# Kernel tuning notes

Measured on AMD Instinct MI355X. Metric: run time of the kernel, lower is better.

## Reference

```python
import jax, jax.numpy as jnp
import numpy as np

B, S, D, H, HD, F = 8, 1024, 512, 8, 64, 2048
EPS = 1e-6

def rmsnorm(x, w):
    var = jnp.mean(x * x, axis=-1, keepdims=True)
    return w * (x * jax.lax.rsqrt(var + EPS))

def setup_inputs() -> dict:
    key = jax.random.key(0)
    ks = jax.random.split(key, 10)
    sd = 512 ** -0.5
    return {
        "primals_1": jax.random.normal(ks[0], (D, D), jnp.float32) * sd,
        "primals_2": jax.random.normal(ks[1], (D, D), jnp.float32) * sd,
        "primals_3": jax.random.normal(ks[2], (D, D), jnp.float32) * sd,
        "primals_4": jax.random.normal(ks[3], (D, D), jnp.float32) * sd,
        "primals_5": jax.random.uniform(ks[4], (D,), jnp.float32, 0.5, 1.5),
        "primals_6": jax.random.normal(ks[5], (F, D), jnp.float32) * sd,
        "primals_7": jax.random.normal(ks[6], (D, F), jnp.float32) * (F ** -0.5),
        "primals_8": jax.random.uniform(ks[7], (D,), jnp.float32, 0.5, 1.5),
        "primals_9": jax.random.normal(ks[8], (B, S, D), jnp.float32),
        "primals_10": jax.random.normal(ks[9], (B, H, S, S), jnp.float32) * 0.1,
    }

def reference(primals_1, primals_2, primals_3, primals_4, primals_5,
              primals_6, primals_7, primals_8, primals_9, primals_10):
    x = primals_9
    # --- self-attention sublayer ---
    h = rmsnorm(x, primals_5)                      # [B,S,D]
    # T5: no 1/sqrt(head_dim) scaling
    q = (h @ primals_3.T).reshape(B, S, H, HD).transpose(0, 2, 1, 3)  # [B,H,S,HD]
    k = (h @ primals_1.T).reshape(B, S, H, HD).transpose(0, 2, 1, 3)
    v = (h @ primals_4.T).reshape(B, S, H, HD).transpose(0, 2, 1, 3)
    scores = jnp.einsum('bhqd,bhkd->bhqk', q, k) + primals_10        # [B,H,S,S]
    attn = jax.nn.softmax(scores, axis=-1)
    ctx = jnp.einsum('bhqk,bhkd->bhqd', attn, v)                     # [B,H,S,HD]
    ctx = ctx.transpose(0, 2, 1, 3).reshape(B, S, D)
    x = x + ctx @ primals_2.T                       # residual add_1
    # --- FFN sublayer ---
    h2 = rmsnorm(x, primals_8)
    ff = jax.nn.relu(h2 @ primals_6.T)              # [B,S,F]
    out = x + ff @ primals_7.T                      # add_3
    return out
```

## Files before the change

### kernel.cpp

```cpp
#include <hip/hip_runtime.h>

#define B_ 8
#define S_ 1024
#define D_ 512
#define H_ 8
#define HD_ 64
#define F_ 2048

typedef unsigned short u16;
typedef unsigned int u32;
typedef __attribute__((ext_vector_type(8))) short bf16x8;
typedef __attribute__((ext_vector_type(4))) float f32x4;

__device__ __forceinline__ float bf2f(u16 u) {
  union { unsigned int i; float f; } v; v.i = ((unsigned int)u) << 16; return v.f;
}
__device__ __forceinline__ u16 f2bf(float f) {
  union { float f; unsigned int i; } v; v.f = f;
  unsigned int r = v.i + 0x7fffu + ((v.i >> 16) & 1u);
  return (u16)(r >> 16);
}

__device__ __forceinline__ void gl2lds16(const u16* g, u16* lds) {
  __builtin_amdgcn_global_load_lds(
      (const __attribute__((address_space(1))) unsigned int*)g,
      (__attribute__((address_space(3))) unsigned int*)lds, 16, 0, 0);
}

__global__ __launch_bounds__(256) void cvt_w_k(const float* __restrict__ wq, const float* __restrict__ wk,
                                               const float* __restrict__ wv, const float* __restrict__ wo,
                                               const float* __restrict__ wf1, const float* __restrict__ wf2,
                                               u16* __restrict__ dst) {
  size_t gid = (size_t)blockIdx.x * 256 + threadIdx.x;
  size_t e0 = gid * 4;
  const float* src; size_t loc;
  if      (e0 <  262144) { src = wq;  loc = e0; }
  else if (e0 <  524288) { src = wk;  loc = e0 -  262144; }
  else if (e0 <  786432) { src = wv;  loc = e0 -  524288; }
  else if (e0 < 1048576) { src = wo;  loc = e0 -  786432; }
  else if (e0 < 2097152) { src = wf1; loc = e0 - 1048576; }
  else                   { src = wf2; loc = e0 - 2097152; }
  float4 v = *(const float4*)(src + loc);
  ushort4 o; o.x = f2bf(v.x); o.y = f2bf(v.y); o.z = f2bf(v.z); o.w = f2bf(v.w);
  *(ushort4*)(dst + e0) = o;
}

template <int IN_BF16>
__global__ __launch_bounds__(256) void rmsnorm_k(const void* __restrict__ xv,
                                                 const float* __restrict__ w,
                                                 u16* __restrict__ out) {
  int row = blockIdx.x;
  int tid = threadIdx.x;
  float x0, x1;
  if (IN_BF16) {
    u32 v = ((const u32*)((const u16*)xv + (size_t)row * D_))[tid];
    x0 = bf2f((u16)(v & 0xffffu)); x1 = bf2f((u16)(v >> 16));
  } else {
    float2 v = ((const float2*)((const float*)xv + (size_t)row * D_))[tid];
    x0 = v.x; x1 = v.y;
  }
  float s = x0 * x0 + x1 * x1;
#pragma unroll
  for (int off = 32; off >= 1; off >>= 1) s += __shfl_xor(s, off, 64);
  __shared__ float red[4];
  int lane = tid & 63, wid = tid >> 6;
  if (lane == 0) red[wid] = s;
  __syncthreads();
  float tot = red[0] + red[1] + red[2] + red[3];
  float inv = rsqrtf(tot * (1.0f / D_) + 1e-6f);
  float2 wv = ((const float2*)w)[tid];
  u32 o = (u32)f2bf(x0 * inv * wv.x) | ((u32)f2bf(x1 * inv * wv.y) << 16);
  ((u32*)(out + (size_t)row * D_))[tid] = o;
}

template <int RELU, int RMODE, int OF32, int BM>
__global__ __launch_bounds__(256) void gemm_mfma_k(const u16* __restrict__ A,
                                                   const u16* __restrict__ W,
                                                   const void* __restrict__ Rv,
                                                   void* __restrict__ Cv,
                                                   int M, int N, int K) {
  constexpr int MI  = BM / 32;
  constexpr int ACH = BM / 16;
  __shared__ __align__(16) u16 As[BM * 32];
  __shared__ __align__(16) u16 Bs[128 * 32];
  int tid = threadIdx.x;
  int w = tid >> 6, l = tid & 63;
  int quad = l >> 4, l16 = l & 15;
  int m0 = blockIdx.y * BM, n0 = blockIdx.x * 128;
  int wr = (w >> 1) * (BM / 2), wc = (w & 1) * 64;

  int c_sw = (l & 3) ^ ((l >> 2) & 3);
  int r_in = l >> 2;
  int swz = quad ^ (l16 & 3);

  f32x4 acc[MI][4];
#pragma unroll
  for (int i = 0; i < MI; i++)
#pragma unroll
    for (int j = 0; j < 4; j++) acc[i][j] = (f32x4)(0.0f);

  for (int k0 = 0; k0 < K; k0 += 32) {
    __syncthreads();
#pragma unroll
    for (int t = 0; t < (ACH + 8) / 4; t++) {
      int ch = w * ((ACH + 8) / 4) + t;
      const u16* src; u16* dst;
      if (ch < ACH) { src = A + (size_t)(m0 + ch * 16 + r_in) * K;         dst = As + ch * 512; }
      else          { src = W + (size_t)(n0 + (ch - ACH) * 16 + r_in) * K; dst = Bs + (ch - ACH) * 512; }
      gl2lds16(src + k0 + c_sw * 8, dst);
    }
    __syncthreads();
    bf16x8 af[MI], bf[4];
#pragma unroll
    for (int i = 0; i < MI; i++)
      af[i] = *(const bf16x8*)(As + (wr + i * 16 + l16) * 32 + swz * 8);
#pragma unroll
    for (int j = 0; j < 4; j++)
      bf[j] = *(const bf16x8*)(Bs + (wc + j * 16 + l16) * 32 + swz * 8);
#pragma unroll
    for (int i = 0; i < MI; i++)
#pragma unroll
      for (int j = 0; j < 4; j++)
        acc[i][j] = __builtin_amdgcn_mfma_f32_16x16x32_bf16(af[i], bf[j], acc[i][j], 0, 0, 0);
  }

#pragma unroll
  for (int i = 0; i < MI; i++)
#pragma unroll
    for (int r = 0; r < 4; r++) {
      int mrow = m0 + wr + i * 16 + quad * 4 + r;
      size_t base = (size_t)mrow * N + n0 + wc + l16;
#pragma unroll
      for (int j = 0; j < 4; j++) {
        float v = acc[i][j][r];
        if (RELU) v = fmaxf(v, 0.0f);
        if (RMODE == 1) v += ((const float*)Rv)[base + j * 16];
        if (RMODE == 2) v += bf2f(((const u16*)Rv)[base + j * 16]);
        if (OF32) ((float*)Cv)[base + j * 16] = v;
        else      ((u16*)Cv)[base + j * 16]   = f2bf(v);
      }
    }
}

__global__ __launch_bounds__(256) void transpose_v_k(const u16* __restrict__ qkv,
                                                     u16* __restrict__ vt) {
  __shared__ u16 T[64][72];
  int t = threadIdx.x;
  int s0 = blockIdx.x * 64, h = blockIdx.y, b = blockIdx.z;
  int skey = t >> 3, dch = (t & 7) * 8;
  int rot = dch >> 3;
#pragma unroll
  for (int rnd = 0; rnd < 2; rnd++) {
    int s = s0 + skey + rnd * 32;
    bf16x8 vv = *(const bf16x8*)(qkv + ((size_t)(b * S_) + s) * 1536 + 1024 + h * HD_ + dch);
#pragma unroll
    for (int i = 0; i < 8; i++) {
      int ii = (i + rot) & 7;
      T[dch + ii][skey + rnd * 32] = (u16)((short*)&vv)[ii];
    }
  }
  __syncthreads();
  int d = t >> 2, kc = (t & 3) * 16;
  bf16x8 a0 = *(const bf16x8*)(&T[d][kc]);
  bf16x8 a1 = *(const bf16x8*)(&T[d][kc + 8]);
  u16* dst = vt + ((size_t)(b * H_ + h) * HD_ + d) * S_ + s0 + kc;
  *(bf16x8*)dst       = a0;
  *(bf16x8*)(dst + 8) = a1;
}

#define FIXED_M 20.0f

__global__ __launch_bounds__(256, 2) void attn_v9_k(const u16* __restrict__ qkv,
                                                    const u16* __restrict__ vt,
                                                    const float* __restrict__ bias,
                                                    u16* __restrict__ ctx) {
  int tid = threadIdx.x;
  int w = tid >> 6, lane = tid & 63;
  int quad = lane >> 4, l16 = lane & 15;
  int h = blockIdx.y, b = blockIdx.z;
  int q0 = blockIdx.x * 64;

  __shared__ __align__(16) u16 KV[2][4 * 2048];
  __shared__ __align__(16) u16 BiasL[2][4][2048];
  __shared__ __align__(16) u16 Pl[4][16 * 72];

  const u16* qrow = qkv + ((size_t)(b * S_) + q0 + w * 16 + l16) * 1536 + h * HD_;
  bf16x8 qf0 = *(const bf16x8*)(qrow + quad * 8);
  bf16x8 qf1 = *(const bf16x8*)(qrow + 32 + quad * 8);

  float lr = 0.0f;
  f32x4 Oacc[4];
#pragma unroll
  for (int nt = 0; nt < 4; nt++) Oacc[nt] = (f32x4)(0.0f);

  const float* brow0 = bias + ((size_t)((b * H_ + h) * S_) + q0 + w * 16) * S_;

  int kv_srow_base = lane >> 2;
  int kv_sc = lane & 3;
  int b_rl_base = lane >> 4;
  int b_p = lane & 15;

  auto stage = [&](u16* kvbuf, u16* bbuf, int kt) {
#pragma unroll
    for (int i = 0; i < 4; i++) {
      int srow = i * 16 + kv_srow_base;
      int slc = kv_sc ^ (srow & 3);
      const u16* src;
      if (w == 0)      src = qkv + ((size_t)(b * S_) + kt + srow) * 1536 + 512 + h * HD_ + slc * 8;
      else if (w == 1) src = qkv + ((size_t)(b * S_) + kt + srow) * 1536 + 544 + h * HD_ + slc * 8;
      else if (w == 2) src = vt + ((size_t)((b * H_ + h) * HD_) + srow) * S_ + kt + slc * 8;
      else             src = vt + ((size_t)((b * H_ + h) * HD_) + srow) * S_ + kt + 32 + slc * 8;
      gl2lds16(src, kvbuf + w * 2048 + i * 512);
    }
#pragma unroll
    for (int i = 0; i < 4; i++) {
      int rl = i * 4 + b_rl_base;
      int c = b_p ^ (rl & 7);
      const float* fsrc = brow0 + (size_t)rl * S_ + kt + c * 4;
      gl2lds16((const u16*)fsrc, bbuf + i * 512);
    }
  };

  stage(&KV[0][0], &BiasL[0][w][0], 0);
  __syncthreads();

  int cur = 0;
#pragma unroll 1
  for (int t = 0; t < 16; t++) {
    int kt = t * 64;
    if (t < 15) stage(&KV[cur ^ 1][0], &BiasL[cur ^ 1][w][0], kt + 64);
    const u16* kvb = &KV[cur][0];
    const u16* bb = &BiasL[cur][w][0];

    f32x4 sg[4];
    __builtin_amdgcn_s_setprio(1);
#pragma unroll
    for (int g = 0; g < 4; g++) {
      int row = g * 16 + l16;
      int sw = quad ^ (row & 3);
      bf16x8 kf0 = *(const bf16x8*)(kvb + row * 32 + sw * 8);
      bf16x8 kf1 = *(const bf16x8*)(kvb + 2048 + row * 32 + sw * 8);
      f32x4 a = (f32x4)(0.0f);
      a = __builtin_amdgcn_mfma_f32_16x16x32_bf16(kf0, qf0, a, 0, 0, 0);
      a = __builtin_amdgcn_mfma_f32_16x16x32_bf16(kf1, qf1, a, 0, 0, 0);
      sg[g] = a;
    }
    __builtin_amdgcn_s_setprio(0);

#pragma unroll
    for (int g = 0; g < 4; g++) {
      f32x4 bf4 = *(const f32x4*)(bb + (size_t)l16 * 128 + ((u32)((g * 4 + quad) ^ (l16 & 7))) * 8);
      float p0 = __expf(sg[g][0] + bf4[0] - FIXED_M);
      float p1 = __expf(sg[g][1] + bf4[1] - FIXED_M);
      float p2 = __expf(sg[g][2] + bf4[2] - FIXED_M);
      float p3 = __expf(sg[g][3] + bf4[3] - FIXED_M);
      lr += (p0 + p1) + (p2 + p3);
      ushort4 pw;
      pw.x = f2bf(p0); pw.y = f2bf(p1); pw.z = f2bf(p2); pw.w = f2bf(p3);
      *(ushort4*)(&Pl[w][l16 * 72 + g * 16 + quad * 4]) = pw;
    }

    bf16x8 pf0 = *(const bf16x8*)(&Pl[w][l16 * 72 + quad * 8]);
    bf16x8 pf1 = *(const bf16x8*)(&Pl[w][l16 * 72 + 32 + quad * 8]);

    __builtin_amdgcn_s_setprio(1);
#pragma unroll
    for (int nt = 0; nt < 4; nt++) {
      int row = nt * 16 + l16;
      int sw = quad ^ (row & 3);
      bf16x8 vf0 = *(const bf16x8*)(kvb + 4096 + row * 32 + sw * 8);
      bf16x8 vf1 = *(const bf16x8*)(kvb + 6144 + row * 32 + sw * 8);
      Oacc[nt] = __builtin_amdgcn_mfma_f32_16x16x32_bf16(pf0, vf0, Oacc[nt], 0, 0, 0);
      Oacc[nt] = __builtin_amdgcn_mfma_f32_16x16x32_bf16(pf1, vf1, Oacc[nt], 0, 0, 0);
    }
    __builtin_amdgcn_s_setprio(0);

    if (t < 15) {
      asm volatile("s_waitcnt vmcnt(0)" ::: "memory");
      __builtin_amdgcn_sched_barrier(0);
      __builtin_amdgcn_s_barrier();
    }
    cur ^= 1;
  }

  float s = lr;
  s += __shfl_xor(s, 16, 64);
  s += __shfl_xor(s, 32, 64);
  size_t obase = ((size_t)(b * S_) + q0 + w * 16) * D_ + h * HD_;
#pragma unroll
  for (int r = 0; r < 4; r++) {
    float inv = 1.0f / __shfl(s, quad * 4 + r, 64);
    int qr = quad * 4 + r;
#pragma unroll
    for (int nt = 0; nt < 4; nt++) {
      ctx[obase + (size_t)qr * D_ + nt * 16 + l16] = f2bf(Oacc[nt][r] * inv);
    }
  }
}

extern "C" void kernel_launch(void* const* d_in, const int* in_sizes, int n_in,
                              void* d_out, int out_size, void* d_ws, size_t ws_size,
                              hipStream_t stream) {
  const float* Wk   = (const float*)d_in[0];
  const float* Wo   = (const float*)d_in[1];
  const float* Wq   = (const float*)d_in[2];
  const float* Wv   = (const float*)d_in[3];
  const float* g1   = (const float*)d_in[4];
  const float* Wf1  = (const float*)d_in[5];
  const float* Wf2  = (const float*)d_in[6];
  const float* g2   = (const float*)d_in[7];
  const float* X    = (const float*)d_in[8];
  const float* bias = (const float*)d_in[9];
  float* out = (float*)d_out;

  const size_t MD = (size_t)B_ * S_ * D_;
  u16* wbf   = (u16*)d_ws;
  u16* Wqkvb = wbf;
  u16* Wob   = wbf +  786432;
  u16* Wf1b  = wbf + 1048576;
  u16* Wf2b  = wbf + 2097152;
  u16* h     = wbf + 3145728;
  u16* qkv   = h + MD;
  u16* vtb   = qkv + 3 * MD;
  u16* ctx   = vtb + MD;
  u16* ff    = ctx + MD;
  u16* x1    = qkv;
  u16* h2    = h;

  dim3 blk(256);
  const int M = B_ * S_;

  cvt_w_k<<<3072, blk, 0, stream>>>(Wq, Wk, Wv, Wo, Wf1, Wf2, wbf);

  rmsnorm_k<0><<<M, blk, 0, stream>>>(X, g1, h);

  dim3 gqkv(1536 / 128, M / 128);
  gemm_mfma_k<0, 0, 0, 128><<<gqkv, blk, 0, stream>>>(h, Wqkvb, nullptr, qkv, M, 1536, D_);

  dim3 gt(S_ / 64, H_, B_);
  transpose_v_k<<<gt, blk, 0, stream>>>(qkv, vtb);

  dim3 ga(S_ / 64, H_, B_);
  attn_v9_k<<<ga, blk, 0, stream>>>(qkv, vtb, bias, ctx);

  dim3 g512(D_ / 128, M / 128);
  gemm_mfma_k<0, 1, 0, 128><<<g512, blk, 0, stream>>>(ctx, Wob, X, x1, M, D_, D_);

  rmsnorm_k<1><<<M, blk, 0, stream>>>(x1, g2, h2);

  dim3 gff1(F_ / 128, M / 128);
  gemm_mfma_k<1, 0, 0, 128><<<gff1, blk, 0, stream>>>(h2, Wf1b, nullptr, ff, M, F_, D_);

  gemm_mfma_k<0, 2, 1, 128><<<g512, blk, 0, stream>>>(ff, Wf2b, x1, out, M, D_, F_);
}
```

Before: 567.9 us.

## Use 128-key attention tiles with shared K/V/bias staging and smaller GEMM M-tiles

The attention kernel now stages 128 keys per iteration instead of 64, so the loop runs 8 times with half as many barriers. All four waves cooperatively load K, V^T and the bias tiles into new XOR-swizzled LDS layouts, and each wave runs two 64-key sub-steps per tile. LDS use rises to about 115 KB per block, so launch bounds drop to one block per CU. The output-projection and FFN2 GEMMs switch to 64-row M tiles, doubling their grid to raise occupancy on the 512-wide outputs.

```diff
diff --git a/kernel.cpp b/kernel.cpp
--- a/kernel.cpp
+++ b/kernel.cpp
@@ -170,18 +170,19 @@
 
 #define FIXED_M 20.0f
 
-__global__ __launch_bounds__(256, 2) void attn_v9_k(const u16* __restrict__ qkv,
-                                                    const u16* __restrict__ vt,
-                                                    const float* __restrict__ bias,
-                                                    u16* __restrict__ ctx) {
+__global__ __launch_bounds__(256, 1) void attn_v10_k(const u16* __restrict__ qkv,
+                                                     const u16* __restrict__ vt,
+                                                     const float* __restrict__ bias,
+                                                     u16* __restrict__ ctx) {
   int tid = threadIdx.x;
   int w = tid >> 6, lane = tid & 63;
   int quad = lane >> 4, l16 = lane & 15;
   int h = blockIdx.y, b = blockIdx.z;
   int q0 = blockIdx.x * 64;
 
-  __shared__ __align__(16) u16 KV[2][4 * 2048];
-  __shared__ __align__(16) u16 BiasL[2][4][2048];
+  __shared__ __align__(16) u16 Ks[2][128 * 64];
+  __shared__ __align__(16) u16 Vs[2][64 * 128];
+  __shared__ __align__(16) u16 Bs[2][64 * 256];
   __shared__ __align__(16) u16 Pl[4][16 * 72];
 
   const u16* qrow = qkv + ((size_t)(b * S_) + q0 + w * 16 + l16) * 1536 + h * HD_;
@@ -193,93 +194,90 @@
 #pragma unroll
   for (int nt = 0; nt < 4; nt++) Oacc[nt] = (f32x4)(0.0f);
 
-  const float* brow0 = bias + ((size_t)((b * H_ + h) * S_) + q0 + w * 16) * S_;
-
-  int kv_srow_base = lane >> 2;
-  int kv_sc = lane & 3;
-  int b_rl_base = lane >> 4;
-  int b_p = lane & 15;
-
-  auto stage = [&](u16* kvbuf, u16* bbuf, int kt) {
+  auto stage = [&](int buf, int kt) {
 #pragma unroll
     for (int i = 0; i < 4; i++) {
-      int srow = i * 16 + kv_srow_base;
-      int slc = kv_sc ^ (srow & 3);
-      const u16* src;
-      if (w == 0)      src = qkv + ((size_t)(b * S_) + kt + srow) * 1536 + 512 + h * HD_ + slc * 8;
-      else if (w == 1) src = qkv + ((size_t)(b * S_) + kt + srow) * 1536 + 544 + h * HD_ + slc * 8;
-      else if (w == 2) src = vt + ((size_t)((b * H_ + h) * HD_) + srow) * S_ + kt + slc * 8;
-      else             src = vt + ((size_t)((b * H_ + h) * HD_) + srow) * S_ + kt + 32 + slc * 8;
-      gl2lds16(src, kvbuf + w * 2048 + i * 512);
+      int j = w * 4 + i;
+      int kr = j * 8 + (lane >> 3);
+      int cs = (lane & 7) ^ (lane >> 3);
+      const u16* src = qkv + ((size_t)(b * S_) + kt + kr) * 1536 + 512 + h * HD_ + cs * 8;
+      gl2lds16(src, &Ks[buf][j * 512]);
     }
 #pragma unroll
     for (int i = 0; i < 4; i++) {
-      int rl = i * 4 + b_rl_base;
-      int c = b_p ^ (rl & 7);
-      const float* fsrc = brow0 + (size_t)rl * S_ + kt + c * 4;
-      gl2lds16((const u16*)fsrc, bbuf + i * 512);
+      int j = w * 4 + i;
+      int vr = j * 4 + (lane >> 4);
+      int cs = (lane & 15) ^ (vr & 7);
+      const u16* src = vt + ((size_t)((b * H_ + h) * HD_) + vr) * S_ + kt + cs * 8;
+      gl2lds16(src, &Vs[buf][j * 512]);
+    }
+#pragma unroll
+    for (int i = 0; i < 8; i++) {
+      int rq = i * 2 + (lane >> 5);
+      int cs = (lane & 31) ^ (rq & 7);
+      const float* fsrc = bias + ((size_t)((b * H_ + h) * S_) + q0 + w * 16 + rq) * S_ + kt + cs * 4;
+      gl2lds16((const u16*)fsrc, &Bs[buf][(w * 16 + i * 2) * 256]);
     }
   };
 
-  stage(&KV[0][0], &BiasL[0][w][0], 0);
+  stage(0, 0);
   __syncthreads();
 
   int cur = 0;
 #pragma unroll 1
-  for (int t = 0; t < 16; t++) {
-    int kt = t * 64;
-    if (t < 15) stage(&KV[cur ^ 1][0], &BiasL[cur ^ 1][w][0], kt + 64);
-    const u16* kvb = &KV[cur][0];
-    const u16* bb = &BiasL[cur][w][0];
-
-    f32x4 sg[4];
-    __builtin_amdgcn_s_setprio(1);
-#pragma unroll
-    for (int g = 0; g < 4; g++) {
-      int row = g * 16 + l16;
-      int sw = quad ^ (row & 3);
-      bf16x8 kf0 = *(const bf16x8*)(kvb + row * 32 + sw * 8);
-      bf16x8 kf1 = *(const bf16x8*)(kvb + 2048 + row * 32 + sw * 8);
-      f32x4 a = (f32x4)(0.0f);
-      a = __builtin_amdgcn_mfma_f32_16x16x32_bf16(kf0, qf0, a, 0, 0, 0);
-      a = __builtin_amdgcn_mfma_f32_16x16x32_bf16(kf1, qf1, a, 0, 0, 0);
-      sg[g] = a;
-    }
-    __builtin_amdgcn_s_setprio(0);
-
-#pragma unroll
-    for (int g = 0; g < 4; g++) {
-      f32x4 bf4 = *(const f32x4*)(bb + (size_t)l16 * 128 + ((u32)((g * 4 + quad) ^ (l16 & 7))) * 8);
-      float p0 = __expf(sg[g][0] + bf4[0] - FIXED_M);
-      float p1 = __expf(sg[g][1] + bf4[1] - FIXED_M);
-      float p2 = __expf(sg[g][2] + bf4[2] - FIXED_M);
-      float p3 = __expf(sg[g][3] + bf4[3] - FIXED_M);
-      lr += (p0 + p1) + (p2 + p3);
-      ushort4 pw;
-      pw.x = f2bf(p0); pw.y = f2bf(p1); pw.z = f2bf(p2); pw.w = f2bf(p3);
-      *(ushort4*)(&Pl[w][l16 * 72 + g * 16 + quad * 4]) = pw;
-    }
-
-    bf16x8 pf0 = *(const bf16x8*)(&Pl[w][l16 * 72 + quad * 8]);
-    bf16x8 pf1 = *(const bf16x8*)(&Pl[w][l16 * 72 + 32 + quad * 8]);
-
-    __builtin_amdgcn_s_setprio(1);
-#pragma unroll
-    for (int nt = 0; nt < 4; nt++) {
-      int row = nt * 16 + l16;
-      int sw = quad ^ (row & 3);
-      bf16x8 vf0 = *(const bf16x8*)(kvb + 4096 + row * 32 + sw * 8);
-      bf16x8 vf1 = *(const bf16x8*)(kvb + 6144 + row * 32 + sw * 8);
-      Oacc[nt] = __builtin_amdgcn_mfma_f32_16x16x32_bf16(pf0, vf0, Oacc[nt], 0, 0, 0);
-      Oacc[nt] = __builtin_amdgcn_mfma_f32_16x16x32_bf16(pf1, vf1, Oacc[nt], 0, 0, 0);
-    }
-    __builtin_amdgcn_s_setprio(0);
-
-    if (t < 15) {
-      asm volatile("s_waitcnt vmcnt(0)" ::: "memory");
-      __builtin_amdgcn_sched_barrier(0);
-      __builtin_amdgcn_s_barrier();
-    }
+  for (int t = 0; t < 8; t++) {
+    int kt = t * 128;
+    if (t < 7) stage(cur ^ 1, kt + 128);
+    const u16* Ksb = &Ks[cur][0];
+    const u16* Vsb = &Vs[cur][0];
+    const float* Bsb = (const float*)&Bs[cur][0];
+
+#pragma unroll
+    for (int s = 0; s < 2; s++) {
+      f32x4 sg[4];
+      __builtin_amdgcn_s_setprio(1);
+#pragma unroll
+      for (int g = 0; g < 4; g++) {
+        int r = s * 64 + g * 16 + l16;
+        bf16x8 kf0 = *(const bf16x8*)(Ksb + r * 64 + ((quad ^ (l16 & 7)) * 8));
+        bf16x8 kf1 = *(const bf16x8*)(Ksb + r * 64 + (((4 + quad) ^ (l16 & 7)) * 8));
+        f32x4 a = (f32x4)(0.0f);
+        a = __builtin_amdgcn_mfma_f32_16x16x32_bf16(kf0, qf0, a, 0, 0, 0);
+        a = __builtin_amdgcn_mfma_f32_16x16x32_bf16(kf1, qf1, a, 0, 0, 0);
+        sg[g] = a;
+      }
+      __builtin_amdgcn_s_setprio(0);
+
+#pragma unroll
+      for (int g = 0; g < 4; g++) {
+        int G = s * 4 + g;
+        f32x4 bf4 = *(const f32x4*)(Bsb + (size_t)(w * 16 + l16) * 128 + (((G * 4 + quad) ^ (l16 & 7)) * 4));
+        float p0 = __expf(sg[g][0] + bf4[0] - FIXED_M);
+        float p1 = __expf(sg[g][1] + bf4[1] - FIXED_M);
+        float p2 = __expf(sg[g][2] + bf4[2] - FIXED_M);
+        float p3 = __expf(sg[g][3] + bf4[3] - FIXED_M);
+        lr += (p0 + p1) + (p2 + p3);
+        ushort4 pw;
+        pw.x = f2bf(p0); pw.y = f2bf(p1); pw.z = f2bf(p2); pw.w = f2bf(p3);
+        *(ushort4*)(&Pl[w][l16 * 72 + g * 16 + quad * 4]) = pw;
+      }
+
+      bf16x8 pf0 = *(const bf16x8*)(&Pl[w][l16 * 72 + quad * 8]);
+      bf16x8 pf1 = *(const bf16x8*)(&Pl[w][l16 * 72 + 32 + quad * 8]);
+
+      __builtin_amdgcn_s_setprio(1);
+#pragma unroll
+      for (int nt = 0; nt < 4; nt++) {
+        int rv = nt * 16 + l16;
+        bf16x8 vf0 = *(const bf16x8*)(Vsb + rv * 128 + (((s * 8 + quad) ^ (l16 & 7)) * 8));
+        bf16x8 vf1 = *(const bf16x8*)(Vsb + rv * 128 + (((s * 8 + 4 + quad) ^ (l16 & 7)) * 8));
+        Oacc[nt] = __builtin_amdgcn_mfma_f32_16x16x32_bf16(pf0, vf0, Oacc[nt], 0, 0, 0);
+        Oacc[nt] = __builtin_amdgcn_mfma_f32_16x16x32_bf16(pf1, vf1, Oacc[nt], 0, 0, 0);
+      }
+      __builtin_amdgcn_s_setprio(0);
+    }
+
+    __syncthreads();
     cur ^= 1;
   }
 
@@ -341,15 +339,15 @@
   transpose_v_k<<<gt, blk, 0, stream>>>(qkv, vtb);
 
   dim3 ga(S_ / 64, H_, B_);
-  attn_v9_k<<<ga, blk, 0, stream>>>(qkv, vtb, bias, ctx);
-
-  dim3 g512(D_ / 128, M / 128);
-  gemm_mfma_k<0, 1, 0, 128><<<g512, blk, 0, stream>>>(ctx, Wob, X, x1, M, D_, D_);
+  attn_v10_k<<<ga, blk, 0, stream>>>(qkv, vtb, bias, ctx);
+
+  dim3 g512b(D_ / 128, M / 64);
+  gemm_mfma_k<0, 1, 0, 64><<<g512b, blk, 0, stream>>>(ctx, Wob, X, x1, M, D_, D_);
 
   rmsnorm_k<1><<<M, blk, 0, stream>>>(x1, g2, h2);
 
   dim3 gff1(F_ / 128, M / 128);
   gemm_mfma_k<1, 0, 0, 128><<<gff1, blk, 0, stream>>>(h2, Wf1b, nullptr, ff, M, F_, D_);
 
-  gemm_mfma_k<0, 2, 1, 128><<<g512, blk, 0, stream>>>(ff, Wf2b, x1, out, M, D_, F_);
-}
+  gemm_mfma_k<0, 2, 1, 64><<<g512b, blk, 0, stream>>>(ff, Wf2b, x1, out, M, D_, F_);
+}
```

After: 557.8 us. Within noise of the previous version (-1.8%).
